# Performance work log

Hardware: AMD Instinct MI355X
Metric: run time of the kernel (lower is better)

Reference implementation:

```python
import jax, jax.numpy as jnp
import numpy as np

D_MODEL = 512
N_HEADS = 8
D_KV = 64
EPS = 1e-6
ROPE_THETA = 10000.0


def _rms_norm(x, w):
    # T5-style RMSNorm: no mean subtraction, no bias, variance in fp32.
    var = jnp.mean(x.astype(jnp.float32) ** 2, axis=-1, keepdims=True)
    return (x * jax.lax.rsqrt(var + EPS)).astype(x.dtype) * w


def _rope_cos_sin(pos, dk):
    # pos: [B, T] int -> cos/sin: [B, 1, T, dk]
    inv_freq = 1.0 / (ROPE_THETA ** (jnp.arange(0, dk, 2, dtype=jnp.float32) / dk))
    ang = pos.astype(jnp.float32)[:, :, None] * inv_freq[None, None, :]  # [B,T,dk/2]
    ang = jnp.concatenate([ang, ang], axis=-1)                            # [B,T,dk]
    return jnp.cos(ang)[:, None], jnp.sin(ang)[:, None]


def _rotate_half(x):
    h = x.shape[-1] // 2
    return jnp.concatenate([-x[..., h:], x[..., :h]], axis=-1)


def _mha(x, mask, wq, wk, wv, wo, pos=None):
    # x: [B, T, D]; mask: [B, H, T, T] additive
    B, T, _ = x.shape
    def proj(w):
        return (x @ w).reshape(B, T, N_HEADS, D_KV).transpose(0, 2, 1, 3)  # [B,H,T,dk]
    q, k, v = proj(wq), proj(wk), proj(wv)
    if pos is not None:
        cos, sin = _rope_cos_sin(pos, D_KV)
        cos, sin = cos.astype(x.dtype), sin.astype(x.dtype)
        q = q * cos + _rotate_half(q) * sin
        k = k * cos + _rotate_half(k) * sin
    scale = 1.0 / np.sqrt(D_KV)
    scores = jnp.einsum('bhqd,bhkd->bhqk', q, k) * scale + mask
    attn = jax.nn.softmax(scores.astype(jnp.float32), axis=-1).astype(scores.dtype)
    out = jnp.einsum('bhqk,bhkd->bhqd', attn, v)
    out = out.transpose(0, 2, 1, 3).reshape(B, T, N_HEADS * D_KV)
    return out @ wo


def setup_inputs() -> dict:
    key = jax.random.key(0)
    ks = jax.random.split(key, 12)
    B, T = 8, 1024
    s = 1.0 / np.sqrt(D_MODEL)
    inp = {
        'h': jax.random.normal(ks[0], (B, T, D_MODEL), dtype=jnp.float32),
        'pos': jnp.broadcast_to(jnp.arange(T, dtype=jnp.int64 if jax.config.jax_enable_x64 else jnp.int32)[None, :], (B, T)),
        't_mask': jnp.zeros((B, N_HEADS, T, T), dtype=jnp.float32),
        'g_mask': jnp.zeros((T, N_HEADS, B, B), dtype=jnp.float32),
        'ln_t_w': jnp.ones((D_MODEL,), dtype=jnp.float32),
        'ln_g_w': jnp.ones((D_MODEL,), dtype=jnp.float32),
    }
    names = ['wq_t', 'wk_t', 'wv_t', 'wo_t', 'wq_g', 'wk_g', 'wv_g', 'wo_g']
    for i, n in enumerate(names):
        inp[n] = jax.random.normal(ks[i + 1], (D_MODEL, D_MODEL), dtype=jnp.float32) * s
    return inp


def reference(h, pos, t_mask, g_mask, ln_t_w, ln_g_w,
              wq_t, wk_t, wv_t, wo_t, wq_g, wk_g, wv_g, wo_g):
    # --- time attention (over T axis, with RoPE) ---
    normed = _rms_norm(h, ln_t_w)
    attn_t = _mha(normed, t_mask, wq_t, wk_t, wv_t, wo_t, pos=pos)
    h = h + attn_t  # dropout p=0 (eval)
    # --- group attention (over B axis, no RoPE) ---
    h = h.transpose(1, 0, 2)  # [T, B, D]
    normed = _rms_norm(h, ln_g_w)
    attn_g = _mha(normed, g_mask, wq_g, wk_g, wv_g, wo_g, pos=None)
    h = h + attn_g
    return h.transpose(1, 0, 2)  # back to [B, T, D]
```

## Files before the change

### kernel.cpp

```cpp
#include <hip/hip_runtime.h>
#include <hip/hip_bf16.h>
#include <math.h>


typedef __bf16 bf16x8 __attribute__((ext_vector_type(8)));
typedef __bf16 bf16x4 __attribute__((ext_vector_type(4)));
typedef float  f32x4  __attribute__((ext_vector_type(4)));

#define LN1E4_OVER_32 0.2878231366242558f

__device__ __forceinline__ void gld16(const void* g, void* l) {
    __builtin_amdgcn_global_load_lds((const __attribute__((address_space(1))) void*)g,
                                     (__attribute__((address_space(3))) void*)l,
                                     16, 0, 0);
}

__device__ __forceinline__ int swz(int r, int q) {
    return r * 32 + (((q + (r >> 1)) & 3) << 3);
}

__global__ __launch_bounds__(256) void prep_k(
    const float* __restrict__ x, const float* __restrict__ wln, __bf16* __restrict__ y,
    const float* w0, const float* w1, const float* w2, const float* w3,
    const float* w4, const float* w5, const float* w6, const float* w7,
    __bf16* qkvT_t, __bf16* oT_t, __bf16* qkvT_g, __bf16* oT_g)
{
    __shared__ float tile[32][33];
    int bid = blockIdx.x;
    if (bid < 2048) {
        int row = bid * 4 + (threadIdx.x >> 6);
        int l = threadIdx.x & 63;
        const float* xr = x + (size_t)row * 512 + l * 8;
        float4 a = *(const float4*)xr;
        float4 b = *(const float4*)(xr + 4);
        float ss = a.x*a.x + a.y*a.y + a.z*a.z + a.w*a.w
                 + b.x*b.x + b.y*b.y + b.z*b.z + b.w*b.w;
        for (int m = 1; m < 64; m <<= 1) ss += __shfl_xor(ss, m);
        float rms = rsqrtf(ss * (1.0f / 512.0f) + 1e-6f);
        float4 wa = *(const float4*)(wln + l * 8);
        float4 wb = *(const float4*)(wln + l * 8 + 4);
        bf16x8 o;
        o[0] = (__bf16)(a.x * rms * wa.x); o[1] = (__bf16)(a.y * rms * wa.y);
        o[2] = (__bf16)(a.z * rms * wa.z); o[3] = (__bf16)(a.w * rms * wa.w);
        o[4] = (__bf16)(b.x * rms * wb.x); o[5] = (__bf16)(b.y * rms * wb.y);
        o[6] = (__bf16)(b.z * rms * wb.z); o[7] = (__bf16)(b.w * rms * wb.w);
        *(bf16x8*)(y + (size_t)row * 512 + l * 8) = o;
        return;
    }
    int bid2 = bid - 2048;
    int mat = bid2 >> 8, rem = bid2 & 255;
    const float* src; __bf16* dst; int rowOff;
    switch (mat) {
        case 0: src=w0; dst=qkvT_t; rowOff=0;    break;
        case 1: src=w1; dst=qkvT_t; rowOff=512;  break;
        case 2: src=w2; dst=qkvT_t; rowOff=1024; break;
        case 3: src=w3; dst=oT_t;   rowOff=0;    break;
        case 4: src=w4; dst=qkvT_g; rowOff=0;    break;
        case 5: src=w5; dst=qkvT_g; rowOff=512;  break;
        case 6: src=w6; dst=qkvT_g; rowOff=1024; break;
        default: src=w7; dst=oT_g;  rowOff=0;    break;
    }
    int n0 = (rem & 15) * 32, k0 = (rem >> 4) * 32;
    int tt = threadIdx.x;
    int kr = tt >> 3, nc = (tt & 7) * 4;
    float4 v = *(const float4*)(src + (size_t)(k0 + kr) * 512 + n0 + nc);
    tile[kr][nc+0] = v.x; tile[kr][nc+1] = v.y; tile[kr][nc+2] = v.z; tile[kr][nc+3] = v.w;
    __syncthreads();
    int nr = tt >> 3, kc = (tt & 7) * 4;
    bf16x4 o;
    o[0] = (__bf16)tile[kc+0][nr]; o[1] = (__bf16)tile[kc+1][nr];
    o[2] = (__bf16)tile[kc+2][nr]; o[3] = (__bf16)tile[kc+3][nr];
    *(bf16x4*)(dst + (size_t)(rowOff + n0 + nr) * 512 + k0 + kc) = o;
}

__global__ __launch_bounds__(256) void rmsnorm_k(
    const float* __restrict__ x, const float* __restrict__ w, __bf16* __restrict__ y)
{
    int row = blockIdx.x * 4 + (threadIdx.x >> 6);
    int l = threadIdx.x & 63;
    const float* xr = x + (size_t)row * 512 + l * 8;
    float4 a = *(const float4*)xr;
    float4 b = *(const float4*)(xr + 4);
    float ss = a.x*a.x + a.y*a.y + a.z*a.z + a.w*a.w
             + b.x*b.x + b.y*b.y + b.z*b.z + b.w*b.w;
    for (int m = 1; m < 64; m <<= 1) ss += __shfl_xor(ss, m);
    float rms = rsqrtf(ss * (1.0f / 512.0f) + 1e-6f);
    float4 wa = *(const float4*)(w + l * 8);
    float4 wb = *(const float4*)(w + l * 8 + 4);
    int orow = (row & 1023) * 8 + (row >> 10);
    bf16x8 o;
    o[0] = (__bf16)(a.x * rms * wa.x); o[1] = (__bf16)(a.y * rms * wa.y);
    o[2] = (__bf16)(a.z * rms * wa.z); o[3] = (__bf16)(a.w * rms * wa.w);
    o[4] = (__bf16)(b.x * rms * wb.x); o[5] = (__bf16)(b.y * rms * wb.y);
    o[6] = (__bf16)(b.z * rms * wb.z); o[7] = (__bf16)(b.w * rms * wb.w);
    *(bf16x8*)(y + (size_t)orow * 512 + l * 8) = o;
}

__global__ __launch_bounds__(256) void gemm_ep(
    const __bf16* __restrict__ A, const __bf16* __restrict__ Bt,
    const int* __restrict__ pos,
    __bf16* __restrict__ o0, __bf16* __restrict__ o1, __bf16* __restrict__ o2,
    int mode)
{
    __shared__ __bf16 smem[8192];
    __bf16* As = smem;
    __bf16* Bs = smem + 4096;
    int tid = threadIdx.x;
    int l = tid & 63, w = tid >> 6;
    int l16 = l & 15, quad = l >> 4;
    int wm = w >> 1, wn = w & 1;
    int mblk = blockIdx.y * 128, nblk = blockIdx.x * 128;
    f32x4 acc[4][4] = {};

    for (int k0 = 0; k0 < 512; k0 += 32) {
        __syncthreads();
        #pragma unroll
        for (int i = 0; i < 2; ++i) {
            int idx = i * 256 + tid;
            int row = idx >> 2;
            int cl = ((idx & 3) + 4 - ((row >> 1) & 3)) & 3;
            gld16(A  + (size_t)(mblk + row) * 512 + k0 + cl * 8, (char*)As + (size_t)idx * 16);
            gld16(Bt + (size_t)(nblk + row) * 512 + k0 + cl * 8, (char*)Bs + (size_t)idx * 16);
        }
        __syncthreads();
        bf16x8 aF[4], bF[4];
        #pragma unroll
        for (int mt = 0; mt < 4; mt++) aF[mt] = *(bf16x8*)(As + swz(wm * 64 + mt * 16 + l16, quad));
        #pragma unroll
        for (int nt = 0; nt < 4; nt++) bF[nt] = *(bf16x8*)(Bs + swz(wn * 64 + nt * 16 + l16, quad));
        #pragma unroll
        for (int mt = 0; mt < 4; mt++)
            #pragma unroll
            for (int nt = 0; nt < 4; nt++)
                acc[mt][nt] = __builtin_amdgcn_mfma_f32_16x16x32_bf16(aF[mt], bF[nt], acc[mt][nt], 0, 0, 0);
    }
    __syncthreads();

    int colbase = nblk + wn * 64;
    __bf16* bw = smem + w * 1536;
    int rbrow = l >> 3, rbch = (l & 7) * 8;

    int mat = colbase >> 9;
    int hh  = (colbase & 511) >> 6;
    __bf16* dst = (mat == 0) ? o0 : (mat == 1) ? o1 : o2;
    bool isQ = (mat == 0), isV = (mat == 2);
    if (mode == 0 && !isV) {
        float f0 = __expf((float)l16        * -LN1E4_OVER_32);
        float f1 = __expf((float)(16 + l16) * -LN1E4_OVER_32);
        #pragma unroll
        for (int mt = 0; mt < 4; mt++) {
            int grow0 = mblk + wm * 64 + mt * 16;
            int b = grow0 >> 10, t0 = grow0 & 1023;
            int4 p4 = *(const int4*)&pos[grow0 + quad * 4];
            const int pa[4] = {p4.x, p4.y, p4.z, p4.w};
            #pragma unroll
            for (int r = 0; r < 4; r++) {
                float p = (float)pa[r];
                #pragma unroll
                for (int nt = 0; nt < 2; nt++) {
                    int i = nt * 16 + l16;
                    float ang = p * (nt ? f1 : f0);
                    float c, s; __sincosf(ang, &s, &c);
                    float x1 = acc[mt][nt][r], x2 = acc[mt][nt + 2][r];
                    float y1 = x1 * c - x2 * s;
                    float y2 = x2 * c + x1 * s;
                    if (isQ) { y1 *= 0.125f; y2 *= 0.125f; }
                    bw[(quad * 4 + r) * 72 + i]      = (__bf16)y1;
                    bw[(quad * 4 + r) * 72 + i + 32] = (__bf16)y2;
                }
            }
            #pragma unroll
            for (int i = 0; i < 2; ++i) {
                int rr = rbrow + i * 8;
                bf16x8 vv = *(bf16x8*)&bw[rr * 72 + rbch];
                *(bf16x8*)&dst[((size_t)(b * 8 + hh) * 1024 + t0 + rr) * 64 + rbch] = vv;
            }
        }
    } else if (mode == 0) {
        #pragma unroll
        for (int mt = 0; mt < 4; mt++) {
            #pragma unroll
            for (int nt = 0; nt < 4; nt++)
                #pragma unroll
                for (int r = 0; r < 4; r++)
                    bw[(nt * 16 + l16) * 24 + quad * 4 + r] = (__bf16)acc[mt][nt][r];
            int grow0 = mblk + wm * 64 + mt * 16;
            int b = grow0 >> 10, t0 = grow0 & 1023;
            #pragma unroll
            for (int i = 0; i < 2; ++i) {
                int li = i * 64 + l;
                int d = li >> 1, t8 = (li & 1) * 8;
                bf16x8 vv = *(bf16x8*)&bw[d * 24 + t8];
                *(bf16x8*)&dst[((size_t)(b * 8 + hh) * 64 + d) * 1024 + t0 + t8] = vv;
            }
        }
    } else {
        #pragma unroll
        for (int mt = 0; mt < 4; mt++) {
            int grow0 = mblk + wm * 64 + mt * 16;
            #pragma unroll
            for (int nt = 0; nt < 4; nt++)
                #pragma unroll
                for (int r = 0; r < 4; r++) {
                    float v = acc[mt][nt][r];
                    if (isQ) v *= 0.125f;
                    bw[(quad * 4 + r) * 72 + nt * 16 + l16] = (__bf16)v;
                }
            #pragma unroll
            for (int i = 0; i < 2; ++i) {
                int rr = rbrow + i * 8;
                int grow = grow0 + rr;
                int t = grow >> 3, bq = grow & 7;
                bf16x8 vv = *(bf16x8*)&bw[rr * 72 + rbch];
                *(bf16x8*)&dst[(((size_t)t * 8 + hh) * 8 + bq) * 64 + rbch] = vv;
            }
        }
    }
}

__global__ __launch_bounds__(256) void gemm_o(
    const __bf16* __restrict__ A, const __bf16* __restrict__ Bt,
    const float* __restrict__ resid, float* __restrict__ outF, int remap)
{
    __shared__ float fsm[4][1088];
    __bf16* As = (__bf16*)fsm;
    __bf16* Bs = As + 2048;
    int tid = threadIdx.x;
    int l = tid & 63, w = tid >> 6;
    int l16 = l & 15, quad = l >> 4;
    int mblk = blockIdx.y * 64, nblk = blockIdx.x * 128;
    f32x4 acc[8] = {};

    for (int k0 = 0; k0 < 512; k0 += 32) {
        __syncthreads();
        {
            int row = tid >> 2;
            int cl = ((tid & 3) + 4 - ((row >> 1) & 3)) & 3;
            gld16(A + (size_t)(mblk + row) * 512 + k0 + cl * 8, (char*)As + (size_t)tid * 16);
        }
        #pragma unroll
        for (int i = 0; i < 2; ++i) {
            int idx = i * 256 + tid;
            int row = idx >> 2;
            int cl = ((idx & 3) + 4 - ((row >> 1) & 3)) & 3;
            gld16(Bt + (size_t)(nblk + row) * 512 + k0 + cl * 8, (char*)Bs + (size_t)idx * 16);
        }
        __syncthreads();
        bf16x8 aF = *(bf16x8*)(As + swz(w * 16 + l16, quad));
        #pragma unroll
        for (int nt = 0; nt < 8; nt++) {
            bf16x8 bF = *(bf16x8*)(Bs + swz(nt * 16 + l16, quad));
            acc[nt] = __builtin_amdgcn_mfma_f32_16x16x32_bf16(aF, bF, acc[nt], 0, 0, 0);
        }
    }
    __syncthreads();

    float* fw = (float*)((char*)fsm + w * 4352);
    int grow0 = mblk + w * 16;
    #pragma unroll
    for (int nh = 0; nh < 2; nh++) {
        #pragma unroll
        for (int nt = 0; nt < 4; nt++)
            #pragma unroll
            for (int r = 0; r < 4; r++)
                fw[(quad * 4 + r) * 68 + nt * 16 + l16] = acc[nh * 4 + nt][r];
        #pragma unroll
        for (int i = 0; i < 4; ++i) {
            int rr = i * 4 + (l >> 4);
            int c4 = (l & 15) * 4;
            f32x4 a4 = *(f32x4*)&fw[rr * 68 + c4];
            int grow = grow0 + rr;
            int orow = remap ? (((grow & 7) << 10) + (grow >> 3)) : grow;
            size_t oi = (size_t)orow * 512 + nblk + nh * 64 + c4;
            f32x4 r4 = *(const f32x4*)&resid[oi];
            r4 += a4;
            *(f32x4*)&outF[oi] = r4;
        }
    }
}

__global__ __launch_bounds__(512) void flash_t(
    const __bf16* __restrict__ q, const __bf16* __restrict__ k,
    const __bf16* __restrict__ vt, const float* __restrict__ tmask,
    __bf16* __restrict__ ctx)
{
    int bh = blockIdx.y;
    int w = threadIdx.x >> 6, l = threadIdx.x & 63;
    int l16 = l & 15, quad = l >> 4;
    int q0 = blockIdx.x * 128 + w * 16;

    __shared__ __bf16 Ks[64 * 72];
    __shared__ __bf16 Vs[64 * 72];
    __shared__ __bf16 Ps[8][16 * 72];

    bf16x8 aQ0, aQ1;
    {
        const __bf16* qp = q + ((size_t)bh * 1024 + q0 + l16) * 64 + quad * 8;
        aQ0 = *(const bf16x8*)qp;
        aQ1 = *(const bf16x8*)(qp + 32);
    }
    f32x4 o[4] = {};
    float l_acc[4] = {0.0f, 0.0f, 0.0f, 0.0f};

    const float* mrow = tmask + (size_t)bh * 1024 * 1024 + (size_t)(q0 + quad * 4) * 1024 + l16;
    float mc[16];
    #pragma unroll
    for (int r = 0; r < 4; r++)
        #pragma unroll
        for (int nt = 0; nt < 4; nt++)
            mc[r * 4 + nt] = __builtin_nontemporal_load(mrow + (size_t)r * 1024 + nt * 16);

    for (int jb = 0; jb < 1024; jb += 64) {
        __syncthreads();
        {
            int c = threadIdx.x;
            int row = c >> 3, col = (c & 7) << 3;
            *(bf16x8*)&Ks[row * 72 + col] = *(const bf16x8*)&k [((size_t)bh * 1024 + jb + row) * 64 + col];
            *(bf16x8*)&Vs[row * 72 + col] = *(const bf16x8*)&vt[((size_t)bh * 64 + row) * 1024 + jb + col];
        }
        __syncthreads();

        float mn_[16];
        {
            int jb2 = (jb + 64) & 1023;
            const float* mr2 = mrow + jb2;
            #pragma unroll
            for (int r = 0; r < 4; r++)
                #pragma unroll
                for (int nt = 0; nt < 4; nt++)
                    mn_[r * 4 + nt] = __builtin_nontemporal_load(mr2 + (size_t)r * 1024 + nt * 16);
        }

        f32x4 s[4] = {};
        #pragma unroll
        for (int nt = 0; nt < 4; nt++) {
            bf16x8 b0 = *(bf16x8*)&Ks[(nt * 16 + l16) * 72 + quad * 8];
            bf16x8 b1 = *(bf16x8*)&Ks[(nt * 16 + l16) * 72 + 32 + quad * 8];
            s[nt] = __builtin_amdgcn_mfma_f32_16x16x32_bf16(aQ0, b0, s[nt], 0, 0, 0);
            s[nt] = __builtin_amdgcn_mfma_f32_16x16x32_bf16(aQ1, b1, s[nt], 0, 0, 0);
        }
        #pragma unroll
        for (int r = 0; r < 4; r++)
            #pragma unroll
            for (int nt = 0; nt < 4; nt++) {
                float p = __expf(s[nt][r] + mc[r * 4 + nt]);
                s[nt][r] = p;
                l_acc[r] += p;
            }

        __bf16* ps = Ps[w];
        #pragma unroll
        for (int nt = 0; nt < 4; nt++)
            #pragma unroll
            for (int r = 0; r < 4; r++)
                ps[(quad * 4 + r) * 72 + nt * 16 + l16] = (__bf16)s[nt][r];
        bf16x8 aP0 = *(bf16x8*)&ps[l16 * 72 + quad * 8];
        bf16x8 aP1 = *(bf16x8*)&ps[l16 * 72 + 32 + quad * 8];
        #pragma unroll
        for (int dt = 0; dt < 4; dt++) {
            bf16x8 bv0 = *(bf16x8*)&Vs[(dt * 16 + l16) * 72 + quad * 8];
            bf16x8 bv1 = *(bf16x8*)&Vs[(dt * 16 + l16) * 72 + 32 + quad * 8];
            o[dt] = __builtin_amdgcn_mfma_f32_16x16x32_bf16(aP0, bv0, o[dt], 0, 0, 0);
            o[dt] = __builtin_amdgcn_mfma_f32_16x16x32_bf16(aP1, bv1, o[dt], 0, 0, 0);
        }

        #pragma unroll
        for (int i = 0; i < 16; i++) mc[i] = mn_[i];
    }

    float l_i[4];
    #pragma unroll
    for (int r = 0; r < 4; r++) {
        float rs = l_acc[r];
        rs += __shfl_xor(rs, 1);
        rs += __shfl_xor(rs, 2);
        rs += __shfl_xor(rs, 4);
        rs += __shfl_xor(rs, 8);
        l_i[r] = rs;
    }

    int b = bh >> 3, h = bh & 7;
    __bf16* ps = Ps[w];
    #pragma unroll
    for (int dt = 0; dt < 4; dt++)
        #pragma unroll
        for (int r = 0; r < 4; r++)
            ps[(quad * 4 + r) * 72 + dt * 16 + l16] = (__bf16)(o[dt][r] / l_i[r]);
    int rbrow = l >> 3, rbch = (l & 7) * 8;
    #pragma unroll
    for (int i = 0; i < 2; ++i) {
        int rr = rbrow + i * 8;
        bf16x8 vv = *(bf16x8*)&ps[rr * 72 + rbch];
        *(bf16x8*)&ctx[((size_t)b * 1024 + q0 + rr) * 512 + h * 64 + rbch] = vv;
    }
}

__global__ __launch_bounds__(256) void group_attn(
    const __bf16* __restrict__ qg, const __bf16* __restrict__ kg,
    const __bf16* __restrict__ vg, const float* __restrict__ gmask,
    __bf16* __restrict__ ctxg)
{
    int tid = blockIdx.x * 256 + threadIdx.x;
    int t = tid >> 6, h = (tid >> 3) & 7, bq = tid & 7;
    size_t base = ((size_t)t * 8 + h) * 512;

    float qv[64];
    #pragma unroll
    for (int d0 = 0; d0 < 64; d0 += 8) {
        bf16x8 qq = *(const bf16x8*)&qg[base + (size_t)bq * 64 + d0];
        #pragma unroll
        for (int u = 0; u < 8; u++) qv[d0 + u] = (float)qq[u];
    }
    float s[8];
    #pragma unroll
    for (int j = 0; j < 8; j++) {
        float acc = 0.0f;
        #pragma unroll
        for (int d0 = 0; d0 < 64; d0 += 8) {
            bf16x8 kk = *(const bf16x8*)&kg[base + (size_t)j * 64 + d0];
            #pragma unroll
            for (int u = 0; u < 8; u++) acc += qv[d0 + u] * (float)kk[u];
        }
        s[j] = acc + gmask[(((size_t)t * 8 + h) * 8 + bq) * 8 + j];
    }
    float mx = s[0];
    #pragma unroll
    for (int j = 1; j < 8; j++) mx = fmaxf(mx, s[j]);
    float sum = 0.0f;
    #pragma unroll
    for (int j = 0; j < 8; j++) { s[j] = __expf(s[j] - mx); sum += s[j]; }
    float inv = 1.0f / sum;

    #pragma unroll
    for (int d0 = 0; d0 < 64; d0 += 8) {
        float o8[8] = {};
        #pragma unroll
        for (int j = 0; j < 8; j++) {
            bf16x8 vv = *(const bf16x8*)&vg[base + (size_t)j * 64 + d0];
            float pj = s[j];
            #pragma unroll
            for (int u = 0; u < 8; u++) o8[u] += pj * (float)vv[u];
        }
        bf16x8 ob;
        #pragma unroll
        for (int u = 0; u < 8; u++) ob[u] = (__bf16)(o8[u] * inv);
        *(bf16x8*)&ctxg[((size_t)t * 8 + bq) * 512 + h * 64 + d0] = ob;
    }
}

extern "C" void kernel_launch(void* const* d_in, const int* in_sizes, int n_in,
                              void* d_out, int out_size, void* d_ws, size_t ws_size,
                              hipStream_t stream)
{
    const float* h      = (const float*)d_in[0];
    const int*   pos    = (const int*)  d_in[1];
    const float* t_mask = (const float*)d_in[2];
    const float* g_mask = (const float*)d_in[3];
    const float* ln_t_w = (const float*)d_in[4];
    const float* ln_g_w = (const float*)d_in[5];
    const float* wq_t = (const float*)d_in[6];
    const float* wk_t = (const float*)d_in[7];
    const float* wv_t = (const float*)d_in[8];
    const float* wo_t = (const float*)d_in[9];
    const float* wq_g = (const float*)d_in[10];
    const float* wk_g = (const float*)d_in[11];
    const float* wv_g = (const float*)d_in[12];
    const float* wo_g = (const float*)d_in[13];
    float* out = (float*)d_out;

    char* ws = (char*)d_ws;
    const size_t MB = 1ull << 20;
    __bf16* qkvT_t = (__bf16*)ws;
    __bf16* oT_t   = qkvT_t + 786432;
    __bf16* qkvT_g = qkvT_t + 1048576;
    __bf16* oT_g   = qkvT_t + 1835008;
    __bf16* normed = (__bf16*)(ws + 4 * MB);
    __bf16* qb     = (__bf16*)(ws + 12 * MB);
    __bf16* kb     = (__bf16*)(ws + 20 * MB);
    __bf16* vb     = (__bf16*)(ws + 28 * MB);
    __bf16* ctx    = (__bf16*)(ws + 36 * MB);
    float*  h2     = (float*) (ws + 44 * MB);

    prep_k<<<4096, 256, 0, stream>>>(h, ln_t_w, normed,
        wq_t, wk_t, wv_t, wo_t, wq_g, wk_g, wv_g, wo_g,
        qkvT_t, oT_t, qkvT_g, oT_g);
    gemm_ep<<<dim3(12, 64), 256, 0, stream>>>(normed, qkvT_t, pos, qb, kb, vb, 0);
    flash_t<<<dim3(8, 64), 512, 0, stream>>>(qb, kb, vb, t_mask, ctx);
    gemm_o<<<dim3(4, 128), 256, 0, stream>>>(ctx, oT_t, h, h2, 0);

    rmsnorm_k<<<2048, 256, 0, stream>>>(h2, ln_g_w, normed);
    gemm_ep<<<dim3(12, 64), 256, 0, stream>>>(normed, qkvT_g, nullptr, qb, kb, vb, 2);
    group_attn<<<256, 256, 0, stream>>>(qb, kb, vb, g_mask, ctx);
    gemm_o<<<dim3(4, 128), 256, 0, stream>>>(ctx, oT_g, h2, out, 1);
}
```

Baseline: 515.0 us.

## Double GEMM K-step to 64 with 8-way swizzle and swap grid axes

Both projection GEMMs now stage 64-wide K slices per iteration instead of 32, using a new 8-chunk XOR-style LDS swizzle. This halves the number of barrier pairs and load rounds in the K loop, at the cost of doubled LDS per block, which may lower occupancy. Grid dimensions are also swapped for the GEMMs and flash attention, so consecutive blocks walk along M (or along heads) rather than N. This changes which blocks share weight or K/V tiles in L2 at the same time.

```diff
diff --git a/kernel.cpp b/kernel.cpp
--- a/kernel.cpp
+++ b/kernel.cpp
@@ -15,8 +15,8 @@
                                      16, 0, 0);
 }
 
-__device__ __forceinline__ int swz(int r, int q) {
-    return r * 32 + (((q + (r >> 1)) & 3) << 3);
+__device__ __forceinline__ int swz64(int r, int c) {
+    return r * 64 + (((c + r) & 7) << 3);
 }
 
 __global__ __launch_bounds__(256) void prep_k(
@@ -102,37 +102,40 @@
     __bf16* __restrict__ o0, __bf16* __restrict__ o1, __bf16* __restrict__ o2,
     int mode)
 {
-    __shared__ __bf16 smem[8192];
+    __shared__ __bf16 smem[16384];
     __bf16* As = smem;
-    __bf16* Bs = smem + 4096;
+    __bf16* Bs = smem + 8192;
     int tid = threadIdx.x;
     int l = tid & 63, w = tid >> 6;
     int l16 = l & 15, quad = l >> 4;
     int wm = w >> 1, wn = w & 1;
-    int mblk = blockIdx.y * 128, nblk = blockIdx.x * 128;
+    int mblk = blockIdx.x * 128, nblk = blockIdx.y * 128;
     f32x4 acc[4][4] = {};
 
-    for (int k0 = 0; k0 < 512; k0 += 32) {
+    for (int k0 = 0; k0 < 512; k0 += 64) {
         __syncthreads();
         #pragma unroll
-        for (int i = 0; i < 2; ++i) {
+        for (int i = 0; i < 4; ++i) {
             int idx = i * 256 + tid;
-            int row = idx >> 2;
-            int cl = ((idx & 3) + 4 - ((row >> 1) & 3)) & 3;
+            int row = idx >> 3, cp = idx & 7;
+            int cl = (cp - row) & 7;
             gld16(A  + (size_t)(mblk + row) * 512 + k0 + cl * 8, (char*)As + (size_t)idx * 16);
             gld16(Bt + (size_t)(nblk + row) * 512 + k0 + cl * 8, (char*)Bs + (size_t)idx * 16);
         }
         __syncthreads();
-        bf16x8 aF[4], bF[4];
-        #pragma unroll
-        for (int mt = 0; mt < 4; mt++) aF[mt] = *(bf16x8*)(As + swz(wm * 64 + mt * 16 + l16, quad));
-        #pragma unroll
-        for (int nt = 0; nt < 4; nt++) bF[nt] = *(bf16x8*)(Bs + swz(wn * 64 + nt * 16 + l16, quad));
-        #pragma unroll
-        for (int mt = 0; mt < 4; mt++)
-            #pragma unroll
-            for (int nt = 0; nt < 4; nt++)
-                acc[mt][nt] = __builtin_amdgcn_mfma_f32_16x16x32_bf16(aF[mt], bF[nt], acc[mt][nt], 0, 0, 0);
+        #pragma unroll
+        for (int h = 0; h < 2; h++) {
+            bf16x8 aF[4], bF[4];
+            #pragma unroll
+            for (int mt = 0; mt < 4; mt++) aF[mt] = *(bf16x8*)(As + swz64(wm * 64 + mt * 16 + l16, h * 4 + quad));
+            #pragma unroll
+            for (int nt = 0; nt < 4; nt++) bF[nt] = *(bf16x8*)(Bs + swz64(wn * 64 + nt * 16 + l16, h * 4 + quad));
+            #pragma unroll
+            for (int mt = 0; mt < 4; mt++)
+                #pragma unroll
+                for (int nt = 0; nt < 4; nt++)
+                    acc[mt][nt] = __builtin_amdgcn_mfma_f32_16x16x32_bf16(aF[mt], bF[nt], acc[mt][nt], 0, 0, 0);
+        }
     }
     __syncthreads();
 
@@ -222,40 +225,45 @@
     const __bf16* __restrict__ A, const __bf16* __restrict__ Bt,
     const float* __restrict__ resid, float* __restrict__ outF, int remap)
 {
-    __shared__ float fsm[4][1088];
-    __bf16* As = (__bf16*)fsm;
-    __bf16* Bs = As + 2048;
+    __shared__ __align__(16) char smemraw[24576];
+    __bf16* As = (__bf16*)smemraw;
+    __bf16* Bs = (__bf16*)(smemraw + 8192);
     int tid = threadIdx.x;
     int l = tid & 63, w = tid >> 6;
     int l16 = l & 15, quad = l >> 4;
-    int mblk = blockIdx.y * 64, nblk = blockIdx.x * 128;
+    int mblk = blockIdx.x * 64, nblk = blockIdx.y * 128;
     f32x4 acc[8] = {};
 
-    for (int k0 = 0; k0 < 512; k0 += 32) {
+    for (int k0 = 0; k0 < 512; k0 += 64) {
         __syncthreads();
-        {
-            int row = tid >> 2;
-            int cl = ((tid & 3) + 4 - ((row >> 1) & 3)) & 3;
-            gld16(A + (size_t)(mblk + row) * 512 + k0 + cl * 8, (char*)As + (size_t)tid * 16);
-        }
         #pragma unroll
         for (int i = 0; i < 2; ++i) {
             int idx = i * 256 + tid;
-            int row = idx >> 2;
-            int cl = ((idx & 3) + 4 - ((row >> 1) & 3)) & 3;
+            int row = idx >> 3, cp = idx & 7;
+            int cl = (cp - row) & 7;
+            gld16(A + (size_t)(mblk + row) * 512 + k0 + cl * 8, (char*)As + (size_t)idx * 16);
+        }
+        #pragma unroll
+        for (int i = 0; i < 4; ++i) {
+            int idx = i * 256 + tid;
+            int row = idx >> 3, cp = idx & 7;
+            int cl = (cp - row) & 7;
             gld16(Bt + (size_t)(nblk + row) * 512 + k0 + cl * 8, (char*)Bs + (size_t)idx * 16);
         }
         __syncthreads();
-        bf16x8 aF = *(bf16x8*)(As + swz(w * 16 + l16, quad));
-        #pragma unroll
-        for (int nt = 0; nt < 8; nt++) {
-            bf16x8 bF = *(bf16x8*)(Bs + swz(nt * 16 + l16, quad));
-            acc[nt] = __builtin_amdgcn_mfma_f32_16x16x32_bf16(aF, bF, acc[nt], 0, 0, 0);
+        #pragma unroll
+        for (int h = 0; h < 2; h++) {
+            bf16x8 aF = *(bf16x8*)(As + swz64(w * 16 + l16, h * 4 + quad));
+            #pragma unroll
+            for (int nt = 0; nt < 8; nt++) {
+                bf16x8 bF = *(bf16x8*)(Bs + swz64(nt * 16 + l16, h * 4 + quad));
+                acc[nt] = __builtin_amdgcn_mfma_f32_16x16x32_bf16(aF, bF, acc[nt], 0, 0, 0);
+            }
         }
     }
     __syncthreads();
 
-    float* fw = (float*)((char*)fsm + w * 4352);
+    float* fw = (float*)(smemraw + w * 4352);
     int grow0 = mblk + w * 16;
     #pragma unroll
     for (int nh = 0; nh < 2; nh++) {
@@ -284,10 +292,10 @@
     const __bf16* __restrict__ vt, const float* __restrict__ tmask,
     __bf16* __restrict__ ctx)
 {
-    int bh = blockIdx.y;
+    int bh = blockIdx.x;
     int w = threadIdx.x >> 6, l = threadIdx.x & 63;
     int l16 = l & 15, quad = l >> 4;
-    int q0 = blockIdx.x * 128 + w * 16;
+    int q0 = blockIdx.y * 128 + w * 16;
 
     __shared__ __bf16 Ks[64 * 72];
     __shared__ __bf16 Vs[64 * 72];
@@ -484,12 +492,12 @@
     prep_k<<<4096, 256, 0, stream>>>(h, ln_t_w, normed,
         wq_t, wk_t, wv_t, wo_t, wq_g, wk_g, wv_g, wo_g,
         qkvT_t, oT_t, qkvT_g, oT_g);
-    gemm_ep<<<dim3(12, 64), 256, 0, stream>>>(normed, qkvT_t, pos, qb, kb, vb, 0);
-    flash_t<<<dim3(8, 64), 512, 0, stream>>>(qb, kb, vb, t_mask, ctx);
-    gemm_o<<<dim3(4, 128), 256, 0, stream>>>(ctx, oT_t, h, h2, 0);
+    gemm_ep<<<dim3(64, 12), 256, 0, stream>>>(normed, qkvT_t, pos, qb, kb, vb, 0);
+    flash_t<<<dim3(64, 8), 512, 0, stream>>>(qb, kb, vb, t_mask, ctx);
+    gemm_o<<<dim3(128, 4), 256, 0, stream>>>(ctx, oT_t, h, h2, 0);
 
     rmsnorm_k<<<2048, 256, 0, stream>>>(h2, ln_g_w, normed);
-    gemm_ep<<<dim3(12, 64), 256, 0, stream>>>(normed, qkvT_g, nullptr, qb, kb, vb, 2);
+    gemm_ep<<<dim3(64, 12), 256, 0, stream>>>(normed, qkvT_g, nullptr, qb, kb, vb, 2);
     group_attn<<<256, 256, 0, stream>>>(qb, kb, vb, g_mask, ctx);
-    gemm_o<<<dim3(4, 128), 256, 0, stream>>>(ctx, oT_g, h2, out, 1);
-}
+    gemm_o<<<dim3(128, 4), 256, 0, stream>>>(ctx, oT_g, h2, out, 1);
+}
```

After: 502.7 us. 1.02x faster.
